# Kernel tuning notes

Hardware: AMD Instinct MI355X
Metric: run time of the kernel (lower is better)

## Reference

```python
import jax, jax.numpy as jnp
import numpy as np
import math

B, C, HLAT, WLON = 1, 256, 46, 90
HEADS = 8
KC = 256   # k_channels (defaults to in_channels)
OC = 256   # out_channels (defaults to in_channels)


def _cc_weights(n):
    # Clenshaw-Curtis quadrature weights on n nodes x_k = cos(k*pi/(n-1)) over [-1, 1]
    # (torch-harmonics 'equiangular' grid quadrature); weights sum to 2.
    N = n - 1
    k = np.arange(n)
    j = np.arange(1, N // 2 + 1)
    b = np.where(2 * j == N, 1.0, 2.0)
    s = (b / (4.0 * j**2 - 1.0))[None, :] * np.cos(2.0 * np.pi * np.outer(k, j) / N)
    w = (1.0 - s.sum(axis=1)) * (2.0 / N)
    w[0] *= 0.5
    w[-1] *= 0.5
    return w


def _log_quad_weights(nlat, nlon):
    wgl = _cc_weights(nlat).astype(np.float32)            # [nlat]
    qw = 2.0 * np.pi * wgl / nlon                          # [nlat]
    qw = np.tile(qw.reshape(-1, 1), (1, nlon)).flatten()   # [nlat*nlon]
    return np.log(qw).reshape(1, 1, -1)                    # (1, 1, N)


def setup_inputs() -> dict:
    key = jax.random.key(0)
    ks = jax.random.split(key, 6)
    scale_qkv = math.sqrt(3.0 / C)
    scale_proj = math.sqrt(3.0 / OC)
    uni = lambda k, shp, s: s * (2.0 * jax.random.uniform(k, shp, dtype=jnp.float32) - 1.0)
    return {
        "query": jax.random.normal(ks[0], (B, C, HLAT, WLON), dtype=jnp.float32),
        "q_w": uni(ks[1], (KC, C), scale_qkv),
        "q_b": jnp.zeros((KC,), dtype=jnp.float32),
        "k_w": uni(ks[2], (KC, C), scale_qkv),
        "k_b": jnp.zeros((KC,), dtype=jnp.float32),
        "v_w": uni(ks[3], (OC, C), scale_qkv),
        "v_b": jnp.zeros((OC,), dtype=jnp.float32),
        "p_w": uni(ks[4], (OC, OC), scale_proj),
        "p_b": jnp.zeros((OC,), dtype=jnp.float32),
        "log_qw": jnp.asarray(_log_quad_weights(HLAT, WLON)),
    }


def _conv1x1(x, w, b):
    # 1x1 conv == per-pixel channel GEMM
    return jnp.einsum("bchw,kc->bkhw", x, w) + b[None, :, None, None]


def _to_seq(x, heads):
    # [B, heads*d, H, W] -> [B, heads, H*W, d]
    b, c, h, w = x.shape
    d = c // heads
    return x.reshape(b, heads, d, h, w).transpose(0, 1, 3, 4, 2).reshape(b, heads, h * w, d)


def reference(query, q_w, q_b, k_w, k_b, v_w, v_b, p_w, p_b, log_qw):
    # key = value = query (self-attention path of the module)
    q = _conv1x1(query, q_w, q_b)
    k = _conv1x1(query, k_w, k_b)
    v = _conv1x1(query, v_w, v_b)

    qs = _to_seq(q, HEADS)   # [B, h, N, dk]
    ks = _to_seq(k, HEADS)   # [B, h, M, dk]
    vs = _to_seq(v, HEADS)   # [B, h, M, dv]

    dk = KC // HEADS
    scale = 1.0 / math.sqrt(dk)  # SDPA default scale
    # scores with additive log-quadrature-weight bias over keys
    scores = jnp.einsum("bhnd,bhmd->bhnm", qs, ks) * scale + log_qw[:, :, None, :]
    attn = jax.nn.softmax(scores, axis=-1)
    out = jnp.einsum("bhnm,bhmd->bhnd", attn, vs)  # [B, h, N, dv]

    bb, hh, nn, dv = out.shape
    out = out.transpose(0, 1, 3, 2).reshape(bb, hh * dv, HLAT, WLON)
    out = _conv1x1(out, p_w, p_b)
    return out
```

## Files before the change

kernel.cpp:

```cpp
#include <hip/hip_runtime.h>

#define N_SEQ 4140
#define NP    4160
#define C_IN  256
#define HEADS 8
#define NT32  130
#define HN    (HEADS * N_SEQ)
#define LOG2E 1.4426950408889634f
#define SCALE2 (0.17677669529663687f * LOG2E)

typedef _Float16 f16x8 __attribute__((ext_vector_type(8)));
typedef _Float16 f16x2 __attribute__((ext_vector_type(2)));
typedef float    f32x16 __attribute__((ext_vector_type(16)));

__device__ inline unsigned short f16b(float x) {
    union { _Float16 h; unsigned short s; } c;
    c.h = (_Float16)x;
    return c.s;
}
__device__ inline f16x2 pkrtz(float a, float b) {
    auto r = __builtin_amdgcn_cvt_pkrtz(a, b);
    union { decltype(r) i; f16x2 o; } c;
    c.i = r;
    return c.o;
}
__device__ inline void permswap(unsigned &a, unsigned &b) {
    asm volatile("v_permlane32_swap_b32 %0, %1" : "+v"(a), "+v"(b));
}

__global__ __launch_bounds__(256) void prep_kernel(
    const float* __restrict__ x, const float* __restrict__ log_qw,
    const float* __restrict__ q_w, const float* __restrict__ k_w,
    const float* __restrict__ v_w, const float* __restrict__ p_w,
    unsigned short* __restrict__ xt, float* __restrict__ lw2,
    unsigned short* __restrict__ wf, unsigned short* __restrict__ pwf)
{
    if (blockIdx.x < NT32) {
        __shared__ unsigned short tile[32][33];
        const int tx = threadIdx.x & 31, ty = threadIdx.x >> 5;
        const int n0 = blockIdx.x * 32, c0 = blockIdx.y * 32;
#pragma unroll
        for (int i = 0; i < 4; ++i) {
            const int c = c0 + ty * 4 + i;
            const int n = n0 + tx;
            const float v = (n < N_SEQ) ? x[(size_t)c * N_SEQ + n] : 0.f;
            tile[tx][ty * 4 + i] = f16b(v);
        }
        __syncthreads();
#pragma unroll
        for (int i = 0; i < 4; ++i) {
            const int nl = ty * 4 + i;
            xt[(size_t)(n0 + nl) * C_IN + c0 + tx] = tile[nl][tx];
        }
    } else {
        const int bid = (blockIdx.x - NT32) * 8 + blockIdx.y;
        for (int i = bid * 256 + threadIdx.x; i < 262144 + NP; i += 24 * 256) {
            if (i < 65536)        wf[i] = f16b(q_w[i] * SCALE2);
            else if (i < 131072)  wf[i] = f16b(k_w[i - 65536]);
            else if (i < 196608)  wf[i] = f16b(v_w[i - 131072]);
            else if (i < 262144)  pwf[i - 196608] = f16b(p_w[i - 196608]);
            else {
                const int j = i - 262144;
                lw2[j] = (j < N_SEQ) ? log_qw[j] * LOG2E : -1e30f;
            }
        }
    }
}

__global__ __launch_bounds__(256) void qkv_mfma(
    const unsigned short* __restrict__ xt, const unsigned short* __restrict__ wf,
    const float* __restrict__ q_b, const float* __restrict__ k_b,
    const float* __restrict__ v_b,
    unsigned short* __restrict__ qo, unsigned short* __restrict__ ko,
    unsigned short* __restrict__ vo)
{
    const int tid = threadIdx.x, wid = tid >> 6, lane = tid & 63;
    const int col = lane & 31, hi = lane >> 5;
    const int w = blockIdx.x * 4 + wid;
    const int ot = w / 65, pt = w % 65;
    const int n0 = pt * 64, n1 = n0 + 32;

    if (ot < 16) {
        const unsigned short* a0 = xt + (size_t)(n0 + col) * C_IN + hi * 8;
        const unsigned short* a1 = xt + (size_t)(n1 + col) * C_IN + hi * 8;
        const unsigned short* bw = wf + (size_t)(ot * 32 + col) * C_IN + hi * 8;
        const float bias = (ot < 8) ? q_b[ot * 32 + col] * SCALE2
                                    : k_b[(ot - 8) * 32 + col];
        f32x16 acc0, acc1;
#pragma unroll
        for (int r = 0; r < 16; ++r) { acc0[r] = bias; acc1[r] = bias; }
#pragma unroll
        for (int t = 0; t < 16; ++t) {
            const f16x8 bf  = *(const f16x8*)(const void*)(bw + t * 16);
            const f16x8 af0 = *(const f16x8*)(const void*)(a0 + t * 16);
            const f16x8 af1 = *(const f16x8*)(const void*)(a1 + t * 16);
            acc0 = __builtin_amdgcn_mfma_f32_32x32x16_f16(af0, bf, acc0, 0, 0, 0);
            acc1 = __builtin_amdgcn_mfma_f32_32x32x16_f16(af1, bf, acc1, 0, 0, 0);
        }
        unsigned short* dst = (ot < 8) ? qo : ko;
        const int h = ot & 7;
#pragma unroll
        for (int r = 0; r < 16; ++r) {
            const int rl = (r & 3) + 8 * (r >> 2) + 4 * hi;
            dst[(size_t)(h * NP + n0 + rl) * 32 + col] = f16b(acc0[r]);
            dst[(size_t)(h * NP + n1 + rl) * 32 + col] = f16b(acc1[r]);
        }
    } else {
        const int h = ot - 16;
        const unsigned short* aw = wf + (size_t)(512 + h * 32 + col) * C_IN + hi * 8;
        const unsigned short* b0 = xt + (size_t)(n0 + col) * C_IN + hi * 8;
        const unsigned short* b1 = xt + (size_t)(n1 + col) * C_IN + hi * 8;
        const float* vb4 = v_b + h * 32 + 4 * hi;
        const float4 c0 = *(const float4*)(vb4);
        const float4 c1 = *(const float4*)(vb4 + 8);
        const float4 c2 = *(const float4*)(vb4 + 16);
        const float4 c3 = *(const float4*)(vb4 + 24);
        f32x16 acc0;
        acc0[0]=c0.x; acc0[1]=c0.y; acc0[2]=c0.z; acc0[3]=c0.w;
        acc0[4]=c1.x; acc0[5]=c1.y; acc0[6]=c1.z; acc0[7]=c1.w;
        acc0[8]=c2.x; acc0[9]=c2.y; acc0[10]=c2.z; acc0[11]=c2.w;
        acc0[12]=c3.x; acc0[13]=c3.y; acc0[14]=c3.z; acc0[15]=c3.w;
        f32x16 acc1 = acc0;
#pragma unroll
        for (int t = 0; t < 16; ++t) {
            const f16x8 af  = *(const f16x8*)(const void*)(aw + t * 16);
            const f16x8 bf0 = *(const f16x8*)(const void*)(b0 + t * 16);
            const f16x8 bf1 = *(const f16x8*)(const void*)(b1 + t * 16);
            acc0 = __builtin_amdgcn_mfma_f32_32x32x16_f16(af, bf0, acc0, 0, 0, 0);
            acc1 = __builtin_amdgcn_mfma_f32_32x32x16_f16(af, bf1, acc1, 0, 0, 0);
        }
        const int nt0 = pt * 2, nt1 = nt0 + 1;
#pragma unroll
        for (int r = 0; r < 16; ++r) {
            const int d = (r & 3) + 8 * (r >> 2) + 4 * hi;
            vo[((size_t)(h * NT32 + nt0) * 32 + d) * 32 + col] = f16b(acc0[r]);
            vo[((size_t)(h * NT32 + nt1) * 32 + d) * 32 + col] = f16b(acc1[r]);
        }
    }
}

__global__ __launch_bounds__(256) void attn_mfma_kernel(
    const unsigned short* __restrict__ qb, const unsigned short* __restrict__ kb,
    const unsigned short* __restrict__ vb, const float* __restrict__ lw2,
    float* __restrict__ pm, float* __restrict__ pl, float* __restrict__ pacc,
    int tiles_per_z)
{
    const int tid = threadIdx.x;
    const int wid = tid >> 6;
    const int lane = tid & 63;
    const int col = lane & 31;
    const int hi = lane >> 5;
    const int job = blockIdx.x * 4 + wid;
    const int h = job / 65;
    const int pt = job % 65;
    const int z = blockIdx.y;

    const int qrowA = pt * 64 + col;
    const int qrowB = qrowA + 32;
    const unsigned short* qpA = qb + ((size_t)(h * NP + qrowA)) * 32 + hi * 8;
    const unsigned short* qpB = qb + ((size_t)(h * NP + qrowB)) * 32 + hi * 8;
    const f16x8 qfA0 = *(const f16x8*)(const void*)(qpA);
    const f16x8 qfA1 = *(const f16x8*)(const void*)(qpA + 16);
    const f16x8 qfB0 = *(const f16x8*)(const void*)(qpB);
    const f16x8 qfB1 = *(const f16x8*)(const void*)(qpB + 16);

    f32x16 oA, oB;
#pragma unroll
    for (int r = 0; r < 16; ++r) { oA[r] = 0.f; oB[r] = 0.f; }
    float mA = -1e30f, lsA = 0.f;
    float mB = -1e30f, lsB = 0.f;
    const f16x2 one2 = { (_Float16)1.f, (_Float16)1.f };

    const int t0 = z * tiles_per_z;
    const int t1 = min(NT32, t0 + tiles_per_z);
    const unsigned short* kbase = kb + (size_t)h * NP * 32;
    const unsigned short* vbase = vb + (size_t)h * NT32 * 1024;

    for (int t = t0; t < t1; ++t) {
        const int k0 = t * 32;
        const unsigned short* kp = kbase + (size_t)(k0 + col) * 32 + hi * 8;
        const f16x8 ka0 = *(const f16x8*)(const void*)(kp);
        const f16x8 ka1 = *(const f16x8*)(const void*)(kp + 16);
        const unsigned short* vp = vbase + (size_t)t * 1024 + col * 32 + hi * 8;
        const f16x8 va0 = *(const f16x8*)(const void*)(vp);
        const f16x8 va1 = *(const f16x8*)(const void*)(vp + 16);

        const float* lw4 = lw2 + k0 + 4 * hi;
        const float4 w0 = *(const float4*)(lw4);
        const float4 w1 = *(const float4*)(lw4 + 8);
        const float4 w2 = *(const float4*)(lw4 + 16);
        const float4 w3 = *(const float4*)(lw4 + 24);
        f32x16 sA;
        sA[0]=w0.x; sA[1]=w0.y; sA[2]=w0.z; sA[3]=w0.w;
        sA[4]=w1.x; sA[5]=w1.y; sA[6]=w1.z; sA[7]=w1.w;
        sA[8]=w2.x; sA[9]=w2.y; sA[10]=w2.z; sA[11]=w2.w;
        sA[12]=w3.x; sA[13]=w3.y; sA[14]=w3.z; sA[15]=w3.w;
        f32x16 sB = sA;

        sA = __builtin_amdgcn_mfma_f32_32x32x16_f16(ka0, qfA0, sA, 0, 0, 0);
        sB = __builtin_amdgcn_mfma_f32_32x32x16_f16(ka0, qfB0, sB, 0, 0, 0);
        sA = __builtin_amdgcn_mfma_f32_32x32x16_f16(ka1, qfA1, sA, 0, 0, 0);
        sB = __builtin_amdgcn_mfma_f32_32x32x16_f16(ka1, qfB1, sB, 0, 0, 0);

        const float a0m = fmaxf(fmaxf(sA[0], sA[1]), sA[2]);
        const float a1m = fmaxf(fmaxf(sA[3], sA[4]), sA[5]);
        const float a2m = fmaxf(fmaxf(sA[6], sA[7]), sA[8]);
        const float a3m = fmaxf(fmaxf(sA[9], sA[10]), sA[11]);
        const float a4m = fmaxf(fmaxf(sA[12], sA[13]), sA[14]);
        const float cmaxA = fmaxf(fmaxf(fmaxf(a0m, a1m), a2m),
                                  fmaxf(fmaxf(a3m, a4m), sA[15]));
        const float b0m = fmaxf(fmaxf(sB[0], sB[1]), sB[2]);
        const float b1m = fmaxf(fmaxf(sB[3], sB[4]), sB[5]);
        const float b2m = fmaxf(fmaxf(sB[6], sB[7]), sB[8]);
        const float b3m = fmaxf(fmaxf(sB[9], sB[10]), sB[11]);
        const float b4m = fmaxf(fmaxf(sB[12], sB[13]), sB[14]);
        const float cmaxB = fmaxf(fmaxf(fmaxf(b0m, b1m), b2m),
                                  fmaxf(fmaxf(b3m, b4m), sB[15]));

        if (!__all(cmaxA - mA <= 8.0f)) {
            float cw = fmaxf(cmaxA, __shfl_xor(cmaxA, 32));
            const float mnew = fmaxf(mA, cw);
            const float esc = __builtin_amdgcn_exp2f(mA - mnew);
            lsA *= esc;
#pragma unroll
            for (int r = 0; r < 16; ++r) oA[r] *= esc;
            mA = mnew;
        }
        if (!__all(cmaxB - mB <= 8.0f)) {
            float cw = fmaxf(cmaxB, __shfl_xor(cmaxB, 32));
            const float mnew = fmaxf(mB, cw);
            const float esc = __builtin_amdgcn_exp2f(mB - mnew);
            lsB *= esc;
#pragma unroll
            for (int r = 0; r < 16; ++r) oB[r] *= esc;
            mB = mnew;
        }

        float pA[16], pB[16];
#pragma unroll
        for (int r = 0; r < 16; ++r) {
            pA[r] = __builtin_amdgcn_exp2f(sA[r] - mA);
            pB[r] = __builtin_amdgcn_exp2f(sB[r] - mB);
        }

        union PK { f16x2 h[4]; unsigned u[4]; f16x8 v; };
        {
            PK k0p, k1p;
            k0p.h[0] = pkrtz(pA[0], pA[1]);
            k0p.h[1] = pkrtz(pA[2], pA[3]);
            k0p.h[2] = pkrtz(pA[4], pA[5]);
            k0p.h[3] = pkrtz(pA[6], pA[7]);
            k1p.h[0] = pkrtz(pA[8], pA[9]);
            k1p.h[1] = pkrtz(pA[10], pA[11]);
            k1p.h[2] = pkrtz(pA[12], pA[13]);
            k1p.h[3] = pkrtz(pA[14], pA[15]);
            float sa = __builtin_amdgcn_fdot2(k0p.h[0], one2, 0.f, false);
            float sb = __builtin_amdgcn_fdot2(k0p.h[1], one2, 0.f, false);
            sa = __builtin_amdgcn_fdot2(k0p.h[2], one2, sa, false);
            sb = __builtin_amdgcn_fdot2(k0p.h[3], one2, sb, false);
            sa = __builtin_amdgcn_fdot2(k1p.h[0], one2, sa, false);
            sb = __builtin_amdgcn_fdot2(k1p.h[1], one2, sb, false);
            sa = __builtin_amdgcn_fdot2(k1p.h[2], one2, sa, false);
            sb = __builtin_amdgcn_fdot2(k1p.h[3], one2, sb, false);
            lsA += sa + sb;
            permswap(k0p.u[0], k0p.u[2]);
            permswap(k0p.u[1], k0p.u[3]);
            oA = __builtin_amdgcn_mfma_f32_32x32x16_f16(va0, k0p.v, oA, 0, 0, 0);
            permswap(k1p.u[0], k1p.u[2]);
            permswap(k1p.u[1], k1p.u[3]);
            oA = __builtin_amdgcn_mfma_f32_32x32x16_f16(va1, k1p.v, oA, 0, 0, 0);
        }
        {
            PK k0p, k1p;
            k0p.h[0] = pkrtz(pB[0], pB[1]);
            k0p.h[1] = pkrtz(pB[2], pB[3]);
            k0p.h[2] = pkrtz(pB[4], pB[5]);
            k0p.h[3] = pkrtz(pB[6], pB[7]);
            k1p.h[0] = pkrtz(pB[8], pB[9]);
            k1p.h[1] = pkrtz(pB[10], pB[11]);
            k1p.h[2] = pkrtz(pB[12], pB[13]);
            k1p.h[3] = pkrtz(pB[14], pB[15]);
            float sa = __builtin_amdgcn_fdot2(k0p.h[0], one2, 0.f, false);
            float sb = __builtin_amdgcn_fdot2(k0p.h[1], one2, 0.f, false);
            sa = __builtin_amdgcn_fdot2(k0p.h[2], one2, sa, false);
            sb = __builtin_amdgcn_fdot2(k0p.h[3], one2, sb, false);
            sa = __builtin_amdgcn_fdot2(k1p.h[0], one2, sa, false);
            sb = __builtin_amdgcn_fdot2(k1p.h[1], one2, sb, false);
            sa = __builtin_amdgcn_fdot2(k1p.h[2], one2, sa, false);
            sb = __builtin_amdgcn_fdot2(k1p.h[3], one2, sb, false);
            lsB += sa + sb;
            permswap(k0p.u[0], k0p.u[2]);
            permswap(k0p.u[1], k0p.u[3]);
            oB = __builtin_amdgcn_mfma_f32_32x32x16_f16(va0, k0p.v, oB, 0, 0, 0);
            permswap(k1p.u[0], k1p.u[2]);
            permswap(k1p.u[1], k1p.u[3]);
            oB = __builtin_amdgcn_mfma_f32_32x32x16_f16(va1, k1p.v, oB, 0, 0, 0);
        }
    }

    lsA += __shfl_xor(lsA, 32);
    lsB += __shfl_xor(lsB, 32);

    if (qrowA < N_SEQ) {
        const size_t qi = (size_t)h * N_SEQ + qrowA;
        if (hi == 0) {
            pm[(size_t)z * HN + qi] = mA;
            pl[(size_t)z * HN + qi] = lsA;
        }
        float* pa = pacc + ((size_t)z * HN + qi) * 32;
#pragma unroll
        for (int r = 0; r < 16; ++r)
            pa[(r & 3) + 8 * (r >> 2) + 4 * hi] = oA[r];
    }
    if (qrowB < N_SEQ) {
        const size_t qi = (size_t)h * N_SEQ + qrowB;
        if (hi == 0) {
            pm[(size_t)z * HN + qi] = mB;
            pl[(size_t)z * HN + qi] = lsB;
        }
        float* pa = pacc + ((size_t)z * HN + qi) * 32;
#pragma unroll
        for (int r = 0; r < 16; ++r)
            pa[(r & 3) + 8 * (r >> 2) + 4 * hi] = oB[r];
    }
}

__global__ __launch_bounds__(256) void merge_kernel(
    const float* __restrict__ pm, const float* __restrict__ pl,
    const float* __restrict__ pacc, unsigned short* __restrict__ at_t, int nz)
{
    const int idx = blockIdx.x * 256 + threadIdx.x;
    if (idx >= HN) return;
    const int h = idx / N_SEQ;
    const int n = idx - h * N_SEQ;

    float mg = pm[idx];
    for (int zz = 1; zz < nz; ++zz) mg = fmaxf(mg, pm[(size_t)zz * HN + idx]);

    float lg = 0.f;
    float acc[32];
#pragma unroll
    for (int d = 0; d < 32; ++d) acc[d] = 0.f;
    for (int zz = 0; zz < nz; ++zz) {
        const float e = exp2f(pm[(size_t)zz * HN + idx] - mg);
        lg += pl[(size_t)zz * HN + idx] * e;
        const float* pa = pacc + ((size_t)zz * HN + idx) * 32;
#pragma unroll
        for (int d = 0; d < 32; ++d) acc[d] = fmaf(pa[d], e, acc[d]);
    }
    const float inv = 1.0f / lg;
    union { unsigned short s[32]; uint4 u[4]; } ph;
#pragma unroll
    for (int d = 0; d < 32; ++d) ph.s[d] = f16b(acc[d] * inv);
    uint4* dst = (uint4*)(at_t + (size_t)n * C_IN + h * 32);
#pragma unroll
    for (int i = 0; i < 4; ++i) dst[i] = ph.u[i];
}

__global__ __launch_bounds__(256) void proj_mfma(
    const unsigned short* __restrict__ at_t, const unsigned short* __restrict__ pwf,
    const float* __restrict__ p_b, float* __restrict__ out)
{
    const int tid = threadIdx.x, wid = tid >> 6, lane = tid & 63;
    const int col = lane & 31, hi = lane >> 5;
    const int tile = blockIdx.x * 4 + wid;
    const int ot = tile / NT32, nt = tile % NT32;
    const int n0 = nt * 32;

    const unsigned short* arow = pwf + (size_t)(ot * 32 + col) * C_IN + hi * 8;
    const unsigned short* brow = at_t + (size_t)(n0 + col) * C_IN + hi * 8;

    const float* pb4 = p_b + ot * 32 + 4 * hi;
    const float4 c0 = *(const float4*)(pb4);
    const float4 c1 = *(const float4*)(pb4 + 8);
    const float4 c2 = *(const float4*)(pb4 + 16);
    const float4 c3 = *(const float4*)(pb4 + 24);
    f32x16 acca, accb;
    acca[0]=c0.x; acca[1]=c0.y; acca[2]=c0.z; acca[3]=c0.w;
    acca[4]=c1.x; acca[5]=c1.y; acca[6]=c1.z; acca[7]=c1.w;
    acca[8]=c2.x; acca[9]=c2.y; acca[10]=c2.z; acca[11]=c2.w;
    acca[12]=c3.x; acca[13]=c3.y; acca[14]=c3.z; acca[15]=c3.w;
#pragma unroll
    for (int r = 0; r < 16; ++r) accb[r] = 0.f;

#pragma unroll
    for (int t = 0; t < 8; ++t) {
        const f16x8 afa = *(const f16x8*)(const void*)(arow + t * 16);
        const f16x8 bfa = *(const f16x8*)(const void*)(brow + t * 16);
        const f16x8 afb = *(const f16x8*)(const void*)(arow + (t + 8) * 16);
        const f16x8 bfb = *(const f16x8*)(const void*)(brow + (t + 8) * 16);
        acca = __builtin_amdgcn_mfma_f32_32x32x16_f16(afa, bfa, acca, 0, 0, 0);
        accb = __builtin_amdgcn_mfma_f32_32x32x16_f16(afb, bfb, accb, 0, 0, 0);
    }

    const int n = n0 + col;
    if (n < N_SEQ) {
#pragma unroll
        for (int r = 0; r < 16; ++r) {
            const int oc = ot * 32 + (r & 3) + 8 * (r >> 2) + 4 * hi;
            out[(size_t)oc * N_SEQ + n] = acca[r] + accb[r];
        }
    }
}

extern "C" void kernel_launch(void* const* d_in, const int* in_sizes, int n_in,
                              void* d_out, int out_size, void* d_ws, size_t ws_size,
                              hipStream_t stream) {
    const float* query  = (const float*)d_in[0];
    const float* q_w    = (const float*)d_in[1];
    const float* q_b    = (const float*)d_in[2];
    const float* k_w    = (const float*)d_in[3];
    const float* k_b    = (const float*)d_in[4];
    const float* v_w    = (const float*)d_in[5];
    const float* v_b    = (const float*)d_in[6];
    const float* p_w    = (const float*)d_in[7];
    const float* p_b    = (const float*)d_in[8];
    const float* log_qw = (const float*)d_in[9];

    const size_t HNP32 = (size_t)HEADS * NP * 32;

    unsigned short* xt  = (unsigned short*)d_ws;
    unsigned short* qb  = xt + (size_t)NP * C_IN;
    unsigned short* kb  = qb + HNP32;
    unsigned short* vb  = kb + HNP32;
    unsigned short* wf  = vb + HNP32;
    unsigned short* pwf = wf + 768 * 256;
    float* lw2 = (float*)(pwf + 256 * 256);
    float* pm  = lw2 + NP;
    unsigned short* at_t = qb;

    const size_t base_bytes = (size_t)((char*)pm - (char*)d_ws);
    const size_t per_z = (size_t)HN * 34 * sizeof(float);
    int nz = 1;
    if      (ws_size >= base_bytes + 8 * per_z) nz = 8;
    else if (ws_size >= base_bytes + 4 * per_z) nz = 4;
    else if (ws_size >= base_bytes + 2 * per_z) nz = 2;
    const int tiles_per_z = (NT32 + nz - 1) / nz;

    float* pl   = pm + (size_t)nz * HN;
    float* pacc = pl + (size_t)nz * HN;

    prep_kernel<<<dim3(NT32 + 3, 8), 256, 0, stream>>>(
        query, log_qw, q_w, k_w, v_w, p_w, xt, lw2, wf, pwf);

    qkv_mfma<<<dim3(390), 256, 0, stream>>>(
        xt, wf, q_b, k_b, v_b, qb, kb, vb);

    attn_mfma_kernel<<<dim3(130, nz), 256, 0, stream>>>(
        qb, kb, vb, lw2, pm, pl, pacc, tiles_per_z);

    merge_kernel<<<dim3((HN + 255) / 256), 256, 0, stream>>>(
        pm, pl, pacc, at_t, nz);

    proj_mfma<<<dim3(260), 256, 0, stream>>>(
        at_t, pwf, p_b, (float*)d_out);
}
```

Measured before the change: 171.6 us.

## Use single-wave blocks and finer work split across QKV, attention, merge, projection

```diff
diff --git a/kernel.cpp b/kernel.cpp
--- a/kernel.cpp
+++ b/kernel.cpp
@@ -67,90 +67,86 @@
     }
 }
 
-__global__ __launch_bounds__(256) void qkv_mfma(
+__global__ __launch_bounds__(64) void qkv_mfma(
     const unsigned short* __restrict__ xt, const unsigned short* __restrict__ wf,
     const float* __restrict__ q_b, const float* __restrict__ k_b,
     const float* __restrict__ v_b,
     unsigned short* __restrict__ qo, unsigned short* __restrict__ ko,
     unsigned short* __restrict__ vo)
 {
-    const int tid = threadIdx.x, wid = tid >> 6, lane = tid & 63;
+    const int lane = threadIdx.x;
     const int col = lane & 31, hi = lane >> 5;
-    const int w = blockIdx.x * 4 + wid;
-    const int ot = w / 65, pt = w % 65;
-    const int n0 = pt * 64, n1 = n0 + 32;
+    const int bid = blockIdx.x;
+    const int ot = bid / NT32, nt = bid % NT32;
+    const int n0 = nt * 32;
 
     if (ot < 16) {
-        const unsigned short* a0 = xt + (size_t)(n0 + col) * C_IN + hi * 8;
-        const unsigned short* a1 = xt + (size_t)(n1 + col) * C_IN + hi * 8;
-        const unsigned short* bw = wf + (size_t)(ot * 32 + col) * C_IN + hi * 8;
+        const unsigned short* arow = xt + (size_t)(n0 + col) * C_IN + hi * 8;
+        const unsigned short* brow = wf + (size_t)(ot * 32 + col) * C_IN + hi * 8;
         const float bias = (ot < 8) ? q_b[ot * 32 + col] * SCALE2
                                     : k_b[(ot - 8) * 32 + col];
         f32x16 acc0, acc1;
 #pragma unroll
-        for (int r = 0; r < 16; ++r) { acc0[r] = bias; acc1[r] = bias; }
-#pragma unroll
-        for (int t = 0; t < 16; ++t) {
-            const f16x8 bf  = *(const f16x8*)(const void*)(bw + t * 16);
-            const f16x8 af0 = *(const f16x8*)(const void*)(a0 + t * 16);
-            const f16x8 af1 = *(const f16x8*)(const void*)(a1 + t * 16);
-            acc0 = __builtin_amdgcn_mfma_f32_32x32x16_f16(af0, bf, acc0, 0, 0, 0);
-            acc1 = __builtin_amdgcn_mfma_f32_32x32x16_f16(af1, bf, acc1, 0, 0, 0);
+        for (int r = 0; r < 16; ++r) { acc0[r] = bias; acc1[r] = 0.f; }
+#pragma unroll
+        for (int t = 0; t < 8; ++t) {
+            const f16x8 af0 = *(const f16x8*)(const void*)(arow + t * 16);
+            const f16x8 bf0 = *(const f16x8*)(const void*)(brow + t * 16);
+            const f16x8 af1 = *(const f16x8*)(const void*)(arow + (t + 8) * 16);
+            const f16x8 bf1 = *(const f16x8*)(const void*)(brow + (t + 8) * 16);
+            acc0 = __builtin_amdgcn_mfma_f32_32x32x16_f16(af0, bf0, acc0, 0, 0, 0);
+            acc1 = __builtin_amdgcn_mfma_f32_32x32x16_f16(af1, bf1, acc1, 0, 0, 0);
         }
         unsigned short* dst = (ot < 8) ? qo : ko;
         const int h = ot & 7;
 #pragma unroll
         for (int r = 0; r < 16; ++r) {
             const int rl = (r & 3) + 8 * (r >> 2) + 4 * hi;
-            dst[(size_t)(h * NP + n0 + rl) * 32 + col] = f16b(acc0[r]);
-            dst[(size_t)(h * NP + n1 + rl) * 32 + col] = f16b(acc1[r]);
+            dst[(size_t)(h * NP + n0 + rl) * 32 + col] = f16b(acc0[r] + acc1[r]);
         }
     } else {
         const int h = ot - 16;
-        const unsigned short* aw = wf + (size_t)(512 + h * 32 + col) * C_IN + hi * 8;
-        const unsigned short* b0 = xt + (size_t)(n0 + col) * C_IN + hi * 8;
-        const unsigned short* b1 = xt + (size_t)(n1 + col) * C_IN + hi * 8;
+        const unsigned short* arow = wf + (size_t)(512 + h * 32 + col) * C_IN + hi * 8;
+        const unsigned short* brow = xt + (size_t)(n0 + col) * C_IN + hi * 8;
         const float* vb4 = v_b + h * 32 + 4 * hi;
         const float4 c0 = *(const float4*)(vb4);
         const float4 c1 = *(const float4*)(vb4 + 8);
         const float4 c2 = *(const float4*)(vb4 + 16);
         const float4 c3 = *(const float4*)(vb4 + 24);
-        f32x16 acc0;
+        f32x16 acc0, acc1;
         acc0[0]=c0.x; acc0[1]=c0.y; acc0[2]=c0.z; acc0[3]=c0.w;
         acc0[4]=c1.x; acc0[5]=c1.y; acc0[6]=c1.z; acc0[7]=c1.w;
         acc0[8]=c2.x; acc0[9]=c2.y; acc0[10]=c2.z; acc0[11]=c2.w;
         acc0[12]=c3.x; acc0[13]=c3.y; acc0[14]=c3.z; acc0[15]=c3.w;
-        f32x16 acc1 = acc0;
-#pragma unroll
-        for (int t = 0; t < 16; ++t) {
-            const f16x8 af  = *(const f16x8*)(const void*)(aw + t * 16);
-            const f16x8 bf0 = *(const f16x8*)(const void*)(b0 + t * 16);
-            const f16x8 bf1 = *(const f16x8*)(const void*)(b1 + t * 16);
-            acc0 = __builtin_amdgcn_mfma_f32_32x32x16_f16(af, bf0, acc0, 0, 0, 0);
-            acc1 = __builtin_amdgcn_mfma_f32_32x32x16_f16(af, bf1, acc1, 0, 0, 0);
-        }
-        const int nt0 = pt * 2, nt1 = nt0 + 1;
+#pragma unroll
+        for (int r = 0; r < 16; ++r) acc1[r] = 0.f;
+#pragma unroll
+        for (int t = 0; t < 8; ++t) {
+            const f16x8 af0 = *(const f16x8*)(const void*)(arow + t * 16);
+            const f16x8 bf0 = *(const f16x8*)(const void*)(brow + t * 16);
+            const f16x8 af1 = *(const f16x8*)(const void*)(arow + (t + 8) * 16);
+            const f16x8 bf1 = *(const f16x8*)(const void*)(brow + (t + 8) * 16);
+            acc0 = __builtin_amdgcn_mfma_f32_32x32x16_f16(af0, bf0, acc0, 0, 0, 0);
+            acc1 = __builtin_amdgcn_mfma_f32_32x32x16_f16(af1, bf1, acc1, 0, 0, 0);
+        }
 #pragma unroll
         for (int r = 0; r < 16; ++r) {
             const int d = (r & 3) + 8 * (r >> 2) + 4 * hi;
-            vo[((size_t)(h * NT32 + nt0) * 32 + d) * 32 + col] = f16b(acc0[r]);
-            vo[((size_t)(h * NT32 + nt1) * 32 + d) * 32 + col] = f16b(acc1[r]);
-        }
-    }
-}
-
-__global__ __launch_bounds__(256) void attn_mfma_kernel(
+            vo[((size_t)(h * NT32 + nt) * 32 + d) * 32 + col] = f16b(acc0[r] + acc1[r]);
+        }
+    }
+}
+
+__global__ __launch_bounds__(64) void attn_mfma_kernel(
     const unsigned short* __restrict__ qb, const unsigned short* __restrict__ kb,
     const unsigned short* __restrict__ vb, const float* __restrict__ lw2,
     float* __restrict__ pm, float* __restrict__ pl, float* __restrict__ pacc,
     int tiles_per_z)
 {
-    const int tid = threadIdx.x;
-    const int wid = tid >> 6;
-    const int lane = tid & 63;
+    const int lane = threadIdx.x;
     const int col = lane & 31;
     const int hi = lane >> 5;
-    const int job = blockIdx.x * 4 + wid;
+    const int job = blockIdx.x;
     const int h = job / 65;
     const int pt = job % 65;
     const int z = blockIdx.y;
@@ -329,8 +325,10 @@
     const float* __restrict__ pm, const float* __restrict__ pl,
     const float* __restrict__ pacc, unsigned short* __restrict__ at_t, int nz)
 {
-    const int idx = blockIdx.x * 256 + threadIdx.x;
-    if (idx >= HN) return;
+    const int gid = blockIdx.x * 256 + threadIdx.x;
+    if (gid >= HN * 4) return;
+    const int idx = gid >> 2;
+    const int sub = gid & 3;
     const int h = idx / N_SEQ;
     const int n = idx - h * N_SEQ;
 
@@ -338,32 +336,30 @@
     for (int zz = 1; zz < nz; ++zz) mg = fmaxf(mg, pm[(size_t)zz * HN + idx]);
 
     float lg = 0.f;
-    float acc[32];
-#pragma unroll
-    for (int d = 0; d < 32; ++d) acc[d] = 0.f;
+    float acc[8];
+#pragma unroll
+    for (int d = 0; d < 8; ++d) acc[d] = 0.f;
     for (int zz = 0; zz < nz; ++zz) {
         const float e = exp2f(pm[(size_t)zz * HN + idx] - mg);
         lg += pl[(size_t)zz * HN + idx] * e;
-        const float* pa = pacc + ((size_t)zz * HN + idx) * 32;
-#pragma unroll
-        for (int d = 0; d < 32; ++d) acc[d] = fmaf(pa[d], e, acc[d]);
+        const float* pa = pacc + ((size_t)zz * HN + idx) * 32 + sub * 8;
+#pragma unroll
+        for (int d = 0; d < 8; ++d) acc[d] = fmaf(pa[d], e, acc[d]);
     }
     const float inv = 1.0f / lg;
-    union { unsigned short s[32]; uint4 u[4]; } ph;
-#pragma unroll
-    for (int d = 0; d < 32; ++d) ph.s[d] = f16b(acc[d] * inv);
-    uint4* dst = (uint4*)(at_t + (size_t)n * C_IN + h * 32);
-#pragma unroll
-    for (int i = 0; i < 4; ++i) dst[i] = ph.u[i];
-}
-
-__global__ __launch_bounds__(256) void proj_mfma(
+    union { unsigned short s[8]; uint4 u; } ph;
+#pragma unroll
+    for (int d = 0; d < 8; ++d) ph.s[d] = f16b(acc[d] * inv);
+    *(uint4*)(at_t + (size_t)n * C_IN + h * 32 + sub * 8) = ph.u;
+}
+
+__global__ __launch_bounds__(64) void proj_mfma(
     const unsigned short* __restrict__ at_t, const unsigned short* __restrict__ pwf,
     const float* __restrict__ p_b, float* __restrict__ out)
 {
-    const int tid = threadIdx.x, wid = tid >> 6, lane = tid & 63;
+    const int lane = threadIdx.x;
     const int col = lane & 31, hi = lane >> 5;
-    const int tile = blockIdx.x * 4 + wid;
+    const int tile = blockIdx.x;
     const int ot = tile / NT32, nt = tile % NT32;
     const int n0 = nt * 32;
 
@@ -443,15 +439,15 @@
     prep_kernel<<<dim3(NT32 + 3, 8), 256, 0, stream>>>(
         query, log_qw, q_w, k_w, v_w, p_w, xt, lw2, wf, pwf);
 
-    qkv_mfma<<<dim3(390), 256, 0, stream>>>(
+    qkv_mfma<<<dim3(3120), 64, 0, stream>>>(
         xt, wf, q_b, k_b, v_b, qb, kb, vb);
 
-    attn_mfma_kernel<<<dim3(130, nz), 256, 0, stream>>>(
+    attn_mfma_kernel<<<dim3(520, nz), 64, 0, stream>>>(
         qb, kb, vb, lw2, pm, pl, pacc, tiles_per_z);
 
-    merge_kernel<<<dim3((HN + 255) / 256), 256, 0, stream>>>(
+    merge_kernel<<<dim3((HN * 4 + 255) / 256), 256, 0, stream>>>(
         pm, pl, pacc, at_t, nz);
 
-    proj_mfma<<<dim3(260), 256, 0, stream>>>(
+    proj_mfma<<<dim3(1040), 64, 0, stream>>>(
         at_t, pwf, p_b, (float*)d_out);
 }
```

New measurement: 164.0 us. -4.4%, faster.
